# Optimization experiments

Hardware: AMD Instinct MI355X
Metric: run time of the kernel (lower is better)

Reference implementation:

```python
import jax, jax.numpy as jnp
import numpy as np

B, N, C, H, P, DP = 2, 512, 384, 12, 4, 128
CH = C // H
SCALE = CH ** -0.5
EPS = 1e-5


def setup_inputs() -> dict:
    key = jax.random.key(0)
    ks = jax.random.split(key, 16)
    w = lambda k, i, o: jax.random.normal(k, (i, o), jnp.float32) * 0.02
    inp = {
        'single': jax.random.normal(ks[0], (B, N, C), jnp.float32),
        'pair': jax.random.normal(ks[1], (B, N, N, DP), jnp.float32),
        'rot': jax.random.normal(ks[2], (B, N, 3, 3), jnp.float32),
        'trans': jax.random.normal(ks[3], (B, N, 3), jnp.float32),
        'mask': jnp.ones((B, N), jnp.float32),
        'Wq': w(ks[4], C, C), 'bq': jnp.zeros((C,)),
        'Wk': w(ks[5], C, C), 'bk': jnp.zeros((C,)),
        'Wv': w(ks[6], C, C), 'bv': jnp.zeros((C,)),
        'Wpb': w(ks[7], DP, H), 'bpb': jnp.zeros((H,)),
        'Wqp': w(ks[8], C, H * P * 3), 'bqp': jnp.zeros((H * P * 3,)),
        'Wkp': w(ks[9], C, H * P * 3), 'bkp': jnp.zeros((H * P * 3,)),
        'Wvp': w(ks[10], C, H * P * 3), 'bvp': jnp.zeros((H * P * 3,)),
        'Wo': w(ks[11], C, C), 'bo': jnp.zeros((C,)),
        'Wpo': w(ks[12], H * P * 3, C), 'bpo': jnp.zeros((C,)),
        'ln_g': jnp.ones((C,)), 'ln_b': jnp.zeros((C,)),
    }
    return inp


def _to_global(pts, rot, trans):
    # pts: [B,N,H,P,3], rot: [B,N,3,3], trans: [B,N,3]
    return jnp.einsum('bnhpd,bnde->bnhpe', pts, rot) + trans[:, :, None, None, :]


def reference(single, pair, rot, trans, mask,
              Wq, bq, Wk, bk, Wv, bv, Wpb, bpb,
              Wqp, bqp, Wkp, bkp, Wvp, bvp,
              Wo, bo, Wpo, bpo, ln_g, ln_b):
    q = (single @ Wq + bq).reshape(B, N, H, CH)
    k = (single @ Wk + bk).reshape(B, N, H, CH)
    v = (single @ Wv + bv).reshape(B, N, H, CH)
    pair_bias = jnp.transpose(pair @ Wpb + bpb, (0, 3, 1, 2))  # [B,H,N,N]

    q_pts = (single @ Wqp + bqp).reshape(B, N, H, P, 3)
    k_pts = (single @ Wkp + bkp).reshape(B, N, H, P, 3)
    qg = _to_global(q_pts, rot, trans)
    kg = _to_global(k_pts, rot, trans)

    q2 = jnp.sum(qg * qg, axis=(3, 4))  # [B,N,H]
    k2 = jnp.sum(kg * kg, axis=(3, 4))
    qk = jnp.einsum('bnhpd,bmhpd->bhnm', qg, kg)
    q2h = jnp.transpose(q2, (0, 2, 1))  # [B,H,N]
    k2h = jnp.transpose(k2, (0, 2, 1))
    point_logits = -0.5 * (q2h[..., :, None] + k2h[..., None, :] - 2.0 * qk) * SCALE

    scalar_logits = jnp.einsum('bnhc,bmhc->bhnm', q, k) * SCALE
    logits = scalar_logits + pair_bias + point_logits

    mask2d = mask[:, None, :, None] * mask[:, None, None, :]  # [B,1,N,N]
    logits = jnp.where(mask2d == 0, -1e9, logits)
    attn = jax.nn.softmax(logits, axis=-1)

    weighted_scalar = jnp.einsum('bhnm,bmhc->bnhc', attn, v).reshape(B, N, C)

    v_pts = (single @ Wvp + bvp).reshape(B, N, H, P, 3)
    vg = _to_global(v_pts, rot, trans)
    weighted_points = jnp.einsum('bhnm,bmhpd->bnhpd', attn, vg).reshape(B, N, H * P * 3)

    point_proj = weighted_points @ Wpo + bpo
    out = (weighted_scalar + point_proj) @ Wo + bo

    x = single + out
    mu = jnp.mean(x, axis=-1, keepdims=True)
    var = jnp.mean((x - mu) ** 2, axis=-1, keepdims=True)
    return (x - mu) * jax.lax.rsqrt(var + EPS) * ln_g + ln_b
```

## Files before the change

### kernel.cpp

```cpp
#include <hip/hip_runtime.h>
#include <hip/hip_bf16.h>

#define Bb   2
#define Nn   512
#define Cc   384
#define Hh   12
#define BN   1024
#define NC1  1584
#define CT1  99
#define SCALE 0.17677669529663687f

typedef __attribute__((ext_vector_type(8))) short short8;
typedef __attribute__((ext_vector_type(4))) float f32x4;

__device__ __forceinline__ unsigned short f2bf(float f){
  union { float f; unsigned u; } v; v.f = f;
  unsigned u = v.u;
  unsigned r = u + 0x7fffu + ((u >> 16) & 1u);
  return (unsigned short)(r >> 16);
}
__device__ __forceinline__ float bf_lo(unsigned u){ union{unsigned u; float f;} v; v.u = u << 16; return v.f; }
__device__ __forceinline__ float bf_hi(unsigned u){ union{unsigned u; float f;} v; v.u = u & 0xffff0000u; return v.f; }
__device__ __forceinline__ unsigned pack2(float a, float b){
  return (unsigned)f2bf(a) | ((unsigned)f2bf(b) << 16);
}

__device__ __forceinline__ void bias_job(const float* __restrict__ pair,
    const float* __restrict__ Wpb, const float* __restrict__ bpb,
    unsigned short* __restrict__ biasf, int jid, int tid)
{
  int l = tid & 63, w = tid >> 6;
  long m0 = (long)jid * 64 + w * 16;
  long m = m0 + (l & 15);
  int kb = (l >> 4) << 3;
  int col = l & 15;
  short8 bf[4];
#pragma unroll
  for (int t = 0; t < 4; ++t){
#pragma unroll
    for (int j = 0; j < 8; ++j){
      int k = t * 32 + kb + j;
      float v = (col < 12) ? Wpb[k * 12 + col] : 0.f;
      bf[t][j] = (short)f2bf(v);
    }
  }
  const float* pr = pair + m * 128 + kb;
  f32x4 acc = {0,0,0,0};
#pragma unroll
  for (int t = 0; t < 4; ++t){
    float4 x0 = *(const float4*)(pr + t * 32);
    float4 x1 = *(const float4*)(pr + t * 32 + 4);
    short8 a;
    a[0] = (short)f2bf(x0.x); a[1] = (short)f2bf(x0.y);
    a[2] = (short)f2bf(x0.z); a[3] = (short)f2bf(x0.w);
    a[4] = (short)f2bf(x1.x); a[5] = (short)f2bf(x1.y);
    a[6] = (short)f2bf(x1.z); a[7] = (short)f2bf(x1.w);
    acc = __builtin_amdgcn_mfma_f32_16x16x32_bf16(a, bf[t], acc, 0, 0, 0);
  }
  int h = col;
  if (h < 12){
    long mr = m0 + ((l >> 4) << 2);
    int b  = (int)(mr >> 18);
    int i  = (int)((mr >> 9) & 511);
    int j  = (int)(mr & 511);
    int jt = j >> 5, f = (j >> 4) & 1, g2 = (j >> 2) & 3;
    int qt = i >> 4, q = i & 15;
    float bb = bpb[h];
    long e16 = (((((long)((b * 12 + h) * 16 + jt) * 32 + qt) * 2 + f) * 64) + (g2 * 16 + q)) * 4;
    uint2 wv; wv.x = pack2(acc[0] + bb, acc[1] + bb); wv.y = pack2(acc[2] + bb, acc[3] + bb);
    *(uint2*)(biasf + e16) = wv;
  }
}

__global__ __launch_bounds__(256) void k1_prep_bias(
    const float* __restrict__ single,
    const float* __restrict__ Wq, const float* __restrict__ Wk, const float* __restrict__ Wv,
    const float* __restrict__ Wqp, const float* __restrict__ Wkp, const float* __restrict__ Wvp,
    const float* __restrict__ bq, const float* __restrict__ bk, const float* __restrict__ bv,
    const float* __restrict__ bqp, const float* __restrict__ bkp, const float* __restrict__ bvp,
    const float* __restrict__ Wpo, const float* __restrict__ Wo,
    const float* __restrict__ pair, const float* __restrict__ Wpb, const float* __restrict__ bpb,
    unsigned short* __restrict__ sbf, unsigned short* __restrict__ wcat, float* __restrict__ bcat,
    unsigned short* __restrict__ wpof, unsigned short* __restrict__ wof,
    unsigned short* __restrict__ wppad, unsigned short* __restrict__ biasf)
{
  int bid = blockIdx.x, tid = threadIdx.x;
  if (bid >= 256){ bias_job(pair, Wpb, bpb, biasf, bid - 256, tid); return; }

  const int n0 = BN * Cc;
  const int n1 = 12 * CT1 * 512;
  const int n4 = NC1;
  const int n5 = 61440;
  const int n6 = 147456;
  const int n7 = BN * 16;
  const int total = n0 + n1 + n4 + n5 + n6 + n7;
  for (int i = bid * 256 + tid; i < total; i += 256 * 256){
    int e = i;
    if (e < n0){ sbf[e] = f2bf(single[e]); continue; }
    e -= n0;
    if (e < n1){
      int j8 = e & 7, l = (e >> 3) & 63, ctt = e >> 9;
      int ct = ctt % CT1, t = ctt / CT1;
      int k = t * 32 + ((l >> 4) << 3) + j8;
      int col = (ct << 4) + (l & 15);
      float v;
      if (col < 1152){
        const float* W = (col < 384) ? Wq : (col < 768 ? Wk : Wv);
        v = W[k * 384 + (col % 384)];
      } else {
        int c2 = col - 1152;
        const float* W = (c2 < 144) ? Wqp : (c2 < 288 ? Wkp : Wvp);
        v = W[k * 144 + (c2 % 144)];
      }
      wcat[e] = f2bf(v); continue;
    }
    e -= n1;
    if (e < n4){
      int col = e; float v;
      if (col < 1152){
        const float* bb = (col < 384) ? bq : (col < 768 ? bk : bv);
        v = bb[col % 384];
      } else {
        int c2 = col - 1152;
        const float* bb = (c2 < 144) ? bqp : (c2 < 288 ? bkp : bvp);
        v = bb[c2 % 144];
      }
      bcat[col] = v; continue;
    }
    e -= n4;
    if (e < n5){
      int j8 = e & 7, l = (e >> 3) & 63, ctt = e >> 9;
      int ct = ctt % 24, t = ctt / 24;
      int k = t * 32 + ((l >> 4) << 3) + j8;
      int col = (ct << 4) + (l & 15);
      wpof[e] = (k < 144) ? f2bf(Wpo[k * 384 + col]) : (unsigned short)0;
      continue;
    }
    e -= n5;
    if (e < n6){
      int j8 = e & 7, l = (e >> 3) & 63, ctt = e >> 9;
      int ct = ctt % 24, t = ctt / 24;
      int k = t * 32 + ((l >> 4) << 3) + j8;
      int col = (ct << 4) + (l & 15);
      wof[e] = f2bf(Wo[k * 384 + col]);
      continue;
    }
    e -= n6;
    { int row = e >> 4, c = e & 15; wppad[row * 160 + 144 + c] = 0; }
  }
}

__global__ __launch_bounds__(256) void k2_proj_bias(
    const unsigned short* __restrict__ sbf, const unsigned short* __restrict__ wcat,
    const float* __restrict__ bcat, float* __restrict__ proj,
    const float* __restrict__ pair, const float* __restrict__ Wpb, const float* __restrict__ bpb,
    unsigned short* __restrict__ biasf)
{
  int bid = blockIdx.x, tid = threadIdx.x;
  if (bid >= 528){ bias_job(pair, Wpb, bpb, biasf, 1024 + (bid - 528), tid); return; }

  int l = tid & 63, w = tid >> 6;
  int bx = bid & 15, by = bid >> 4;
  int m0 = bx * 64 + w * 16;
  const unsigned short* Ap = sbf + (long)(m0 + (l & 15)) * Cc + ((l >> 4) << 3);
  int ct0 = by * 3;
  f32x4 acc0 = {0,0,0,0}, acc1 = {0,0,0,0}, acc2 = {0,0,0,0};
  for (int t = 0; t < 12; ++t){
    short8 a = *(const short8*)(Ap + t * 32);
    const unsigned short* wp_ = wcat + ((long)(t * CT1 + ct0) * 64 + l) * 8;
    short8 b0 = *(const short8*)(wp_);
    short8 b1 = *(const short8*)(wp_ + 512);
    short8 b2 = *(const short8*)(wp_ + 1024);
    acc0 = __builtin_amdgcn_mfma_f32_16x16x32_bf16(a, b0, acc0, 0, 0, 0);
    acc1 = __builtin_amdgcn_mfma_f32_16x16x32_bf16(a, b1, acc1, 0, 0, 0);
    acc2 = __builtin_amdgcn_mfma_f32_16x16x32_bf16(a, b2, acc2, 0, 0, 0);
  }
  int rbase = m0 + ((l >> 4) << 2);
  int cb = by * 48 + (l & 15);
#pragma unroll
  for (int c = 0; c < 3; ++c){
    f32x4 ac = (c == 0) ? acc0 : (c == 1 ? acc1 : acc2);
    int col = cb + c * 16;
    float bb = bcat[col];
#pragma unroll
    for (int r = 0; r < 4; ++r)
      proj[(long)(rbase + r) * NC1 + col] = ac[r] + bb;
  }
}

__global__ __launch_bounds__(256) void k3_pack_bias(
    const float* __restrict__ proj, const float* __restrict__ rot,
    const float* __restrict__ trans, const float* __restrict__ mask,
    unsigned short* __restrict__ qf, unsigned short* __restrict__ kf,
    unsigned short* __restrict__ vf, float* __restrict__ q2h, float* __restrict__ k2h,
    const float* __restrict__ pair, const float* __restrict__ Wpb, const float* __restrict__ bpb,
    unsigned short* __restrict__ biasf)
{
  __shared__ float smemf[5792];
  int bid = blockIdx.x, tid = threadIdx.x;
  if (bid >= 384){ bias_job(pair, Wpb, bpb, biasf, 4096 + (bid - 384), tid); return; }

  float* scal = smemf;
  float* praw = scal + 3072;
  float* pg   = praw + 1152;
  float* rots = pg + 1152;
  float* trs  = rots + 288;
  float* msk  = trs + 96;

  int jid = bid;
  int b = jid / 192, rem = jid % 192;
  int h = rem >> 4, rt = rem & 15;
  int j0 = rt * 32;
  int bn0 = b * 512 + j0;
  int bh = b * 12 + h;

  for (int idx = tid; idx < 3072; idx += 256){
    int a = idx >> 10, row = (idx >> 5) & 31, c = idx & 31;
    scal[idx] = proj[(long)(bn0 + row) * NC1 + a * 384 + h * 32 + c];
  }
  for (int idx = tid; idx < 1152; idx += 256){
    int a = idx / 384, rr = idx % 384, row = rr / 12, pe = rr % 12;
    praw[idx] = proj[(long)(bn0 + row) * NC1 + 1152 + a * 144 + h * 12 + pe];
  }
  for (int idx = tid; idx < 288; idx += 256) rots[idx] = rot[(long)bn0 * 9 + idx];
  for (int idx = tid; idx < 96; idx += 256)  trs[idx] = trans[(long)bn0 * 3 + idx];
  for (int idx = tid; idx < 32; idx += 256)  msk[idx] = mask[bn0 + idx];
  __syncthreads();

  for (int idx = tid; idx < 1152; idx += 256){
    int a = idx / 384, rr = idx % 384, row = rr / 12, pe = rr % 12;
    int p = pe / 3, ee = pe % 3;
    pg[idx] = praw[a * 384 + row * 12 + p * 3] * rots[row * 9 + ee]
            + praw[a * 384 + row * 12 + p * 3 + 1] * rots[row * 9 + 3 + ee]
            + praw[a * 384 + row * 12 + p * 3 + 2] * rots[row * 9 + 6 + ee] + trs[row * 3 + ee];
  }
  __syncthreads();

  for (int idx = tid; idx < 64; idx += 256){
    int a = idx >> 5, row = idx & 31;
    float s2 = 0.f;
#pragma unroll
    for (int pe = 0; pe < 12; ++pe){ float g = pg[a * 384 + row * 12 + pe]; s2 += g * g; }
    float mv = msk[row];
    float rres = -0.5f * SCALE * s2 + (mv != 0.f ? 0.f : -2e9f);
    (a ? k2h : q2h)[(long)bh * 512 + j0 + row] = rres;
  }

  for (int idx = tid; idx < 2048; idx += 256){
    int a = idx >> 10, r = idx & 1023;
    int jjp = r & 3, l = (r >> 2) & 63, ks = (r >> 8) & 1, sub = r >> 9;
    int row = sub * 16 + (l & 15);
    int kk = ks * 32 + ((l >> 4) << 3) + jjp * 2;
    int k1 = kk + 1;
    float v0 = (kk < 32) ? scal[a * 1024 + row * 32 + kk] : (kk < 44 ? pg[a * 384 + row * 12 + kk - 32] : 0.f);
    float v1 = (k1 < 32) ? scal[a * 1024 + row * 32 + k1] : (k1 < 44 ? pg[a * 384 + row * 12 + k1 - 32] : 0.f);
    if (a == 0){ v0 *= SCALE; v1 *= SCALE; }
    unsigned* dst = (unsigned*)(a ? kf : qf);
    dst[((((long)bh * 32 + rt * 2 + sub) * 2 + ks) * 64 + l) * 4 + jjp] = pack2(v0, v1);
  }

  for (int idx = tid; idx < 768; idx += 256){
    int jjp = idx & 3, l = (idx >> 2) & 63, cf = idx >> 8;
    int c = cf * 16 + (l & 15);
    int j = ((l >> 4) << 3) + jjp * 2;
    float v0 = (c < 32) ? scal[2048 + j * 32 + c]       : (c < 44 ? pg[768 + j * 12 + (c - 32)]       : 0.f);
    float v1 = (c < 32) ? scal[2048 + (j + 1) * 32 + c] : (c < 44 ? pg[768 + (j + 1) * 12 + (c - 32)] : 0.f);
    ((unsigned*)vf)[(((long)bh * 16 + rt) * 3 + cf) * 256 + l * 4 + jjp] = pack2(v0, v1);
  }
}

__global__ __launch_bounds__(256) void attn2_kernel(
    const unsigned short* __restrict__ qf, const unsigned short* __restrict__ kf,
    const unsigned short* __restrict__ vf, const unsigned short* __restrict__ biasf,
    const float* __restrict__ q2h, const float* __restrict__ k2h,
    float* __restrict__ wsout, unsigned short* __restrict__ wpout)
{
  __shared__ unsigned short pls[4][16][40];
  __shared__ float oW[4][3][64][4];
  __shared__ float mW[4][16], lsW[4][16];
  __shared__ float fW[4][16], linvS[16];

  int l = threadIdx.x & 63, w = threadIdx.x >> 6;
  int qt = blockIdx.x, h = blockIdx.y, b = blockIdx.z;
  int bh = b * 12 + h;
  int g = l >> 4, q_ = l & 15;

  const short8* qp = (const short8*)(qf + (((long)(bh * 32 + qt) * 2) * 64 + l) * 8);
  short8 qA = qp[0], qB = qp[64];
  float cq = q2h[(long)bh * 512 + qt * 16 + q_];

  float m = -1e30f, ls = 0.f;
  f32x4 o0 = {0,0,0,0}, o1 = {0,0,0,0}, o2 = {0,0,0,0};
  const f32x4 z4 = {0,0,0,0};

#pragma unroll
  for (int ji = 0; ji < 4; ++ji){
    int jt = w * 4 + ji;
    const short8* kp = (const short8*)(kf + (((long)(bh * 32 + jt * 2) * 2) * 64 + l) * 8);
    short8 k00 = kp[0], k01 = kp[64], k10 = kp[128], k11 = kp[192];
    f32x4 s0 = __builtin_amdgcn_mfma_f32_16x16x32_bf16(k00, qA, z4, 0, 0, 0);
    s0 = __builtin_amdgcn_mfma_f32_16x16x32_bf16(k01, qB, s0, 0, 0, 0);
    f32x4 s1 = __builtin_amdgcn_mfma_f32_16x16x32_bf16(k10, qA, z4, 0, 0, 0);
    s1 = __builtin_amdgcn_mfma_f32_16x16x32_bf16(k11, qB, s1, 0, 0, 0);

    const uint2* bp = (const uint2*)(biasf + ((((long)(bh * 16 + jt) * 32 + qt) * 2) * 64) * 4);
    uint2 bb0 = bp[l], bb1 = bp[64 + l];
    const float4* k2p = (const float4*)(k2h + (long)bh * 512 + jt * 32);
    float4 ck0 = k2p[g], ck1 = k2p[4 + g];

    s0[0] += bf_lo(bb0.x) + cq + ck0.x;
    s0[1] += bf_hi(bb0.x) + cq + ck0.y;
    s0[2] += bf_lo(bb0.y) + cq + ck0.z;
    s0[3] += bf_hi(bb0.y) + cq + ck0.w;
    s1[0] += bf_lo(bb1.x) + cq + ck1.x;
    s1[1] += bf_hi(bb1.x) + cq + ck1.y;
    s1[2] += bf_lo(bb1.y) + cq + ck1.z;
    s1[3] += bf_hi(bb1.y) + cq + ck1.w;

    float tm = fmaxf(fmaxf(fmaxf(s0[0], s0[1]), fmaxf(s0[2], s0[3])),
                     fmaxf(fmaxf(s1[0], s1[1]), fmaxf(s1[2], s1[3])));
    tm = fmaxf(tm, __shfl_xor(tm, 16));
    tm = fmaxf(tm, __shfl_xor(tm, 32));
    float mn = fmaxf(m, tm);
    float alpha = __expf(m - mn);
    f32x4 p0, p1;
    float ts = 0.f;
#pragma unroll
    for (int r = 0; r < 4; ++r){ p0[r] = __expf(s0[r] - mn); ts += p0[r]; }
#pragma unroll
    for (int r = 0; r < 4; ++r){ p1[r] = __expf(s1[r] - mn); ts += p1[r]; }
    ts += __shfl_xor(ts, 16);
    ts += __shfl_xor(ts, 32);
    ls = ls * alpha + ts; m = mn;

    f32x4 av;
#pragma unroll
    for (int r = 0; r < 4; ++r) av[r] = __shfl(alpha, g * 4 + r);
#pragma unroll
    for (int r = 0; r < 4; ++r){ o0[r] *= av[r]; o1[r] *= av[r]; o2[r] *= av[r]; }

    uint2 w0; w0.x = pack2(p0[0], p0[1]); w0.y = pack2(p0[2], p0[3]);
    uint2 w1; w1.x = pack2(p1[0], p1[1]); w1.y = pack2(p1[2], p1[3]);
    *(uint2*)&pls[w][q_][g * 4]      = w0;
    *(uint2*)&pls[w][q_][16 + g * 4] = w1;
    short8 pa = *(const short8*)&pls[w][q_][g * 8];

    const short8* vp = (const short8*)(vf + (((long)(bh * 16 + jt) * 3) * 64 + l) * 8);
    short8 v0 = vp[0], v1 = vp[64], v2 = vp[128];
    o0 = __builtin_amdgcn_mfma_f32_16x16x32_bf16(pa, v0, o0, 0, 0, 0);
    o1 = __builtin_amdgcn_mfma_f32_16x16x32_bf16(pa, v1, o1, 0, 0, 0);
    o2 = __builtin_amdgcn_mfma_f32_16x16x32_bf16(pa, v2, o2, 0, 0, 0);
  }

  if (g == 0){ mW[w][q_] = m; lsW[w][q_] = ls; }
  *(f32x4*)&oW[w][0][l][0] = o0;
  *(f32x4*)&oW[w][1][l][0] = o1;
  *(f32x4*)&oW[w][2][l][0] = o2;
  __syncthreads();

  if (w == 0){
    float M = fmaxf(fmaxf(mW[0][q_], mW[1][q_]), fmaxf(mW[2][q_], mW[3][q_]));
    float f = __expf(mW[g][q_] - M);
    fW[g][q_] = f;
    float lf = lsW[g][q_] * f;
    lf += __shfl_xor(lf, 16);
    lf += __shfl_xor(lf, 32);
    if (g == 0) linvS[q_] = 1.f / lf;
  }
  __syncthreads();

  if (w < 3){
    float fr[4][4], li[4];
#pragma unroll
    for (int r = 0; r < 4; ++r){
      int q = g * 4 + r;
      li[r] = linvS[q];
#pragma unroll
      for (int vw = 0; vw < 4; ++vw) fr[vw][r] = fW[vw][q];
    }
    f32x4 sum = {0,0,0,0};
#pragma unroll
    for (int vw = 0; vw < 4; ++vw){
      f32x4 ov = *(const f32x4*)&oW[vw][w][l][0];
#pragma unroll
      for (int r = 0; r < 4; ++r) sum[r] += ov[r] * fr[vw][r];
    }
#pragma unroll
    for (int r = 0; r < 4; ++r){
      long bn = (long)b * 512 + qt * 16 + g * 4 + r;
      float val = sum[r] * li[r];
      if (w == 0)      wsout[bn * 384 + h * 32 + q_] = val;
      else if (w == 1) wsout[bn * 384 + h * 32 + 16 + q_] = val;
      else if (q_ < 12) wpout[bn * 160 + h * 12 + q_] = f2bf(val);
    }
  }
}

__global__ __launch_bounds__(256) void tail_kernel(
    const unsigned short* __restrict__ wpbuf, const unsigned short* __restrict__ wpof,
    const float* __restrict__ bpo, const float* __restrict__ wso,
    const unsigned short* __restrict__ wof, const float* __restrict__ bo,
    const float* __restrict__ single, const float* __restrict__ ln_g,
    const float* __restrict__ ln_b, float* __restrict__ out)
{
  __shared__ unsigned short t1s[16][392];
  __shared__ float redS[4][16], redQ[4][16];
  int l = threadIdx.x & 63, w = threadIdx.x >> 6;
  int m0 = blockIdx.x * 16;
  int rb = (l >> 4) << 2;
  int arow = m0 + (l & 15);

  {
    short8 awp[5];
    const unsigned short* Ap = wpbuf + (long)arow * 160 + ((l >> 4) << 3);
#pragma unroll
    for (int t = 0; t < 5; ++t) awp[t] = *(const short8*)(Ap + t * 32);
#pragma unroll
    for (int c6 = 0; c6 < 6; ++c6){
      int ct = w * 6 + c6;
      f32x4 acc = {0,0,0,0};
#pragma unroll
      for (int t = 0; t < 5; ++t){
        short8 bfr = *(const short8*)(wpof + ((long)(t * 24 + ct) * 64 + l) * 8);
        acc = __builtin_amdgcn_mfma_f32_16x16x32_bf16(awp[t], bfr, acc, 0, 0, 0);
      }
      int col = ct * 16 + (l & 15);
      float bb = bpo[col];
#pragma unroll
      for (int r = 0; r < 4; ++r){
        float v = acc[r] + bb + wso[(long)(m0 + rb + r) * 384 + col];
        t1s[rb + r][col] = f2bf(v);
      }
    }
  }
  __syncthreads();

  short8 a2[12];
  {
    int lr = l & 15;
#pragma unroll
    for (int t = 0; t < 12; ++t)
      a2[t] = *(const short8*)&t1s[lr][t * 32 + ((l >> 4) << 3)];
  }
  f32x4 xa[6];
  float s1[4] = {0,0,0,0}, s2[4] = {0,0,0,0};
#pragma unroll
  for (int c6 = 0; c6 < 6; ++c6){
    int ct = w * 6 + c6;
    f32x4 acc = {0,0,0,0};
#pragma unroll
    for (int t = 0; t < 12; ++t){
      short8 bfr = *(const short8*)(wof + ((long)(t * 24 + ct) * 64 + l) * 8);
      acc = __builtin_amdgcn_mfma_f32_16x16x32_bf16(a2[t], bfr, acc, 0, 0, 0);
    }
    int col = ct * 16 + (l & 15);
    float bb = bo[col];
#pragma unroll
    for (int r = 0; r < 4; ++r){
      float v = acc[r] + bb + single[(long)(m0 + rb + r) * 384 + col];
      acc[r] = v; s1[r] += v; s2[r] += v * v;
    }
    xa[c6] = acc;
  }
#pragma unroll
  for (int off = 1; off < 16; off <<= 1){
#pragma unroll
    for (int r = 0; r < 4; ++r){
      s1[r] += __shfl_xor(s1[r], off);
      s2[r] += __shfl_xor(s2[r], off);
    }
  }
  if ((l & 15) == 0){
#pragma unroll
    for (int r = 0; r < 4; ++r){ redS[w][rb + r] = s1[r]; redQ[w][rb + r] = s2[r]; }
  }
  __syncthreads();
  float mu[4], inv[4];
#pragma unroll
  for (int r = 0; r < 4; ++r){
    float ts = redS[0][rb + r] + redS[1][rb + r] + redS[2][rb + r] + redS[3][rb + r];
    float tq = redQ[0][rb + r] + redQ[1][rb + r] + redQ[2][rb + r] + redQ[3][rb + r];
    mu[r] = ts * (1.f / 384.f);
    float var = tq * (1.f / 384.f) - mu[r] * mu[r];
    inv[r] = rsqrtf(var + 1e-5f);
  }
#pragma unroll
  for (int c6 = 0; c6 < 6; ++c6){
    int ct = w * 6 + c6;
    int col = ct * 16 + (l & 15);
    float g = ln_g[col], bt = ln_b[col];
#pragma unroll
    for (int r = 0; r < 4; ++r)
      out[(long)(m0 + rb + r) * 384 + col] = (xa[c6][r] - mu[r]) * inv[r] * g + bt;
  }
}

extern "C" void kernel_launch(void* const* d_in, const int* in_sizes, int n_in,
                              void* d_out, int out_size, void* d_ws, size_t ws_size,
                              hipStream_t stream)
{
  const float* single = (const float*)d_in[0];
  const float* pair   = (const float*)d_in[1];
  const float* rot    = (const float*)d_in[2];
  const float* trans  = (const float*)d_in[3];
  const float* mask   = (const float*)d_in[4];
  const float* Wq  = (const float*)d_in[5];  const float* bq  = (const float*)d_in[6];
  const float* Wk  = (const float*)d_in[7];  const float* bk  = (const float*)d_in[8];
  const float* Wv  = (const float*)d_in[9];  const float* bv  = (const float*)d_in[10];
  const float* Wpb = (const float*)d_in[11]; const float* bpb = (const float*)d_in[12];
  const float* Wqp = (const float*)d_in[13]; const float* bqp = (const float*)d_in[14];
  const float* Wkp = (const float*)d_in[15]; const float* bkp = (const float*)d_in[16];
  const float* Wvp = (const float*)d_in[17]; const float* bvp = (const float*)d_in[18];
  const float* Wo  = (const float*)d_in[19]; const float* bo  = (const float*)d_in[20];
  const float* Wpo = (const float*)d_in[21]; const float* bpo = (const float*)d_in[22];
  const float* ln_g = (const float*)d_in[23]; const float* ln_b = (const float*)d_in[24];

  char* wsb = (char*)d_ws;
  size_t off = 0;
  auto alloc = [&](size_t bytes) -> void* {
    void* p = wsb + off; off += (bytes + 255) & ~(size_t)255; return p;
  };
  unsigned short* sbf  = (unsigned short*)alloc((size_t)BN * Cc * 2);
  unsigned short* wcat = (unsigned short*)alloc((size_t)12 * CT1 * 512 * 2);
  unsigned short* wpof = (unsigned short*)alloc((size_t)5 * 24 * 512 * 2);
  unsigned short* wof  = (unsigned short*)alloc((size_t)12 * 24 * 512 * 2);
  float* bcat  = (float*)alloc(NC1 * 4);
  float* proj  = (float*)alloc((size_t)BN * NC1 * 4);
  unsigned short* biasf = (unsigned short*)alloc((size_t)Bb * Hh * Nn * Nn * 2);
  unsigned short* qfragb = (unsigned short*)alloc((size_t)786432 * 2);
  unsigned short* kfragb = (unsigned short*)alloc((size_t)786432 * 2);
  unsigned short* vfragb = (unsigned short*)alloc((size_t)589824 * 2);
  float* q2hb  = (float*)alloc((size_t)12288 * 4);
  float* k2hb  = (float*)alloc((size_t)12288 * 4);
  float* wso   = (float*)alloc((size_t)BN * 384 * 4);
  unsigned short* wpbuf = (unsigned short*)alloc((size_t)BN * 160 * 2);
  if (off > ws_size) return;

  k1_prep_bias<<<256 + 1024, 256, 0, stream>>>(
      single, Wq, Wk, Wv, Wqp, Wkp, Wvp, bq, bk, bv, bqp, bkp, bvp, Wpo, Wo,
      pair, Wpb, bpb, sbf, wcat, bcat, wpof, wof, wpbuf, biasf);
  k2_proj_bias<<<528 + 3072, 256, 0, stream>>>(
      sbf, wcat, bcat, proj, pair, Wpb, bpb, biasf);
  k3_pack_bias<<<384 + 4096, 256, 0, stream>>>(
      proj, rot, trans, mask, qfragb, kfragb, vfragb, q2hb, k2hb,
      pair, Wpb, bpb, biasf);
  attn2_kernel<<<dim3(32, 12, 2), 256, 0, stream>>>(qfragb, kfragb, vfragb, biasf,
                                                    q2hb, k2hb, wso, wpbuf);
  tail_kernel<<<64, 256, 0, stream>>>(wpbuf, wpof, bpo, wso, wof, bo,
                                      single, ln_g, ln_b, (float*)d_out);
}
```

Before: 106.2 us.

## Fuse pair-bias projection into split-KV attention with merged tail reduction

The pair-bias projection no longer runs as extra blocks in the prep kernels and is no longer staged through a global bf16 bias buffer. It is computed inside the attention kernel per (batch, query tile, 64-key chunk) and kept in LDS, where all 12 heads consume it. Attention is split across 8 key chunks, each writing partial outputs with its max and sum, and the tail kernel merges these flash-style before the output projection and layernorm. This removes a large global round trip of the bias tensor, but the partials buffer adds extra traffic and the merge step adds per-thread register pressure.

New measurement: 133.3 us. 25.5% more time.

```diff
diff --git a/kernel.cpp b/kernel.cpp
--- a/kernel.cpp
+++ b/kernel.cpp
@@ -25,75 +25,23 @@
   return (unsigned)f2bf(a) | ((unsigned)f2bf(b) << 16);
 }
 
-__device__ __forceinline__ void bias_job(const float* __restrict__ pair,
-    const float* __restrict__ Wpb, const float* __restrict__ bpb,
-    unsigned short* __restrict__ biasf, int jid, int tid)
-{
-  int l = tid & 63, w = tid >> 6;
-  long m0 = (long)jid * 64 + w * 16;
-  long m = m0 + (l & 15);
-  int kb = (l >> 4) << 3;
-  int col = l & 15;
-  short8 bf[4];
-#pragma unroll
-  for (int t = 0; t < 4; ++t){
-#pragma unroll
-    for (int j = 0; j < 8; ++j){
-      int k = t * 32 + kb + j;
-      float v = (col < 12) ? Wpb[k * 12 + col] : 0.f;
-      bf[t][j] = (short)f2bf(v);
-    }
-  }
-  const float* pr = pair + m * 128 + kb;
-  f32x4 acc = {0,0,0,0};
-#pragma unroll
-  for (int t = 0; t < 4; ++t){
-    float4 x0 = *(const float4*)(pr + t * 32);
-    float4 x1 = *(const float4*)(pr + t * 32 + 4);
-    short8 a;
-    a[0] = (short)f2bf(x0.x); a[1] = (short)f2bf(x0.y);
-    a[2] = (short)f2bf(x0.z); a[3] = (short)f2bf(x0.w);
-    a[4] = (short)f2bf(x1.x); a[5] = (short)f2bf(x1.y);
-    a[6] = (short)f2bf(x1.z); a[7] = (short)f2bf(x1.w);
-    acc = __builtin_amdgcn_mfma_f32_16x16x32_bf16(a, bf[t], acc, 0, 0, 0);
-  }
-  int h = col;
-  if (h < 12){
-    long mr = m0 + ((l >> 4) << 2);
-    int b  = (int)(mr >> 18);
-    int i  = (int)((mr >> 9) & 511);
-    int j  = (int)(mr & 511);
-    int jt = j >> 5, f = (j >> 4) & 1, g2 = (j >> 2) & 3;
-    int qt = i >> 4, q = i & 15;
-    float bb = bpb[h];
-    long e16 = (((((long)((b * 12 + h) * 16 + jt) * 32 + qt) * 2 + f) * 64) + (g2 * 16 + q)) * 4;
-    uint2 wv; wv.x = pack2(acc[0] + bb, acc[1] + bb); wv.y = pack2(acc[2] + bb, acc[3] + bb);
-    *(uint2*)(biasf + e16) = wv;
-  }
-}
-
-__global__ __launch_bounds__(256) void k1_prep_bias(
+__global__ __launch_bounds__(256) void k1_prep(
     const float* __restrict__ single,
     const float* __restrict__ Wq, const float* __restrict__ Wk, const float* __restrict__ Wv,
     const float* __restrict__ Wqp, const float* __restrict__ Wkp, const float* __restrict__ Wvp,
     const float* __restrict__ bq, const float* __restrict__ bk, const float* __restrict__ bv,
     const float* __restrict__ bqp, const float* __restrict__ bkp, const float* __restrict__ bvp,
     const float* __restrict__ Wpo, const float* __restrict__ Wo,
-    const float* __restrict__ pair, const float* __restrict__ Wpb, const float* __restrict__ bpb,
     unsigned short* __restrict__ sbf, unsigned short* __restrict__ wcat, float* __restrict__ bcat,
-    unsigned short* __restrict__ wpof, unsigned short* __restrict__ wof,
-    unsigned short* __restrict__ wppad, unsigned short* __restrict__ biasf)
+    unsigned short* __restrict__ wpof, unsigned short* __restrict__ wof)
 {
   int bid = blockIdx.x, tid = threadIdx.x;
-  if (bid >= 256){ bias_job(pair, Wpb, bpb, biasf, bid - 256, tid); return; }
-
   const int n0 = BN * Cc;
   const int n1 = 12 * CT1 * 512;
   const int n4 = NC1;
   const int n5 = 61440;
   const int n6 = 147456;
-  const int n7 = BN * 16;
-  const int total = n0 + n1 + n4 + n5 + n6 + n7;
+  const int total = n0 + n1 + n4 + n5 + n6;
   for (int i = bid * 256 + tid; i < total; i += 256 * 256){
     int e = i;
     if (e < n0){ sbf[e] = f2bf(single[e]); continue; }
@@ -137,28 +85,21 @@
       continue;
     }
     e -= n5;
-    if (e < n6){
+    {
       int j8 = e & 7, l = (e >> 3) & 63, ctt = e >> 9;
       int ct = ctt % 24, t = ctt / 24;
       int k = t * 32 + ((l >> 4) << 3) + j8;
       int col = (ct << 4) + (l & 15);
       wof[e] = f2bf(Wo[k * 384 + col]);
-      continue;
-    }
-    e -= n6;
-    { int row = e >> 4, c = e & 15; wppad[row * 160 + 144 + c] = 0; }
-  }
-}
-
-__global__ __launch_bounds__(256) void k2_proj_bias(
+    }
+  }
+}
+
+__global__ __launch_bounds__(256) void k2_proj(
     const unsigned short* __restrict__ sbf, const unsigned short* __restrict__ wcat,
-    const float* __restrict__ bcat, float* __restrict__ proj,
-    const float* __restrict__ pair, const float* __restrict__ Wpb, const float* __restrict__ bpb,
-    unsigned short* __restrict__ biasf)
+    const float* __restrict__ bcat, float* __restrict__ proj)
 {
   int bid = blockIdx.x, tid = threadIdx.x;
-  if (bid >= 528){ bias_job(pair, Wpb, bpb, biasf, 1024 + (bid - 528), tid); return; }
-
   int l = tid & 63, w = tid >> 6;
   int bx = bid & 15, by = bid >> 4;
   int m0 = bx * 64 + w * 16;
@@ -188,17 +129,14 @@
   }
 }
 
-__global__ __launch_bounds__(256) void k3_pack_bias(
+__global__ __launch_bounds__(256) void k3_pack(
     const float* __restrict__ proj, const float* __restrict__ rot,
     const float* __restrict__ trans, const float* __restrict__ mask,
     unsigned short* __restrict__ qf, unsigned short* __restrict__ kf,
-    unsigned short* __restrict__ vf, float* __restrict__ q2h, float* __restrict__ k2h,
-    const float* __restrict__ pair, const float* __restrict__ Wpb, const float* __restrict__ bpb,
-    unsigned short* __restrict__ biasf)
+    unsigned short* __restrict__ vf, float* __restrict__ q2h, float* __restrict__ k2h)
 {
   __shared__ float smemf[5792];
   int bid = blockIdx.x, tid = threadIdx.x;
-  if (bid >= 384){ bias_job(pair, Wpb, bpb, biasf, 4096 + (bid - 384), tid); return; }
 
   float* scal = smemf;
   float* praw = scal + 3072;
@@ -269,150 +207,191 @@
   }
 }
 
-__global__ __launch_bounds__(256) void attn2_kernel(
+__global__ __launch_bounds__(512) void kC_bias_attn(
+    const float* __restrict__ pair, const float* __restrict__ Wpb,
+    const float* __restrict__ bpb,
     const unsigned short* __restrict__ qf, const unsigned short* __restrict__ kf,
-    const unsigned short* __restrict__ vf, const unsigned short* __restrict__ biasf,
+    const unsigned short* __restrict__ vf,
     const float* __restrict__ q2h, const float* __restrict__ k2h,
-    float* __restrict__ wsout, unsigned short* __restrict__ wpout)
+    float* __restrict__ partials)
 {
-  __shared__ unsigned short pls[4][16][40];
-  __shared__ float oW[4][3][64][4];
-  __shared__ float mW[4][16], lsW[4][16];
-  __shared__ float fW[4][16], linvS[16];
-
-  int l = threadIdx.x & 63, w = threadIdx.x >> 6;
-  int qt = blockIdx.x, h = blockIdx.y, b = blockIdx.z;
-  int bh = b * 12 + h;
-  int g = l >> 4, q_ = l & 15;
-
-  const short8* qp = (const short8*)(qf + (((long)(bh * 32 + qt) * 2) * 64 + l) * 8);
-  short8 qA = qp[0], qB = qp[64];
-  float cq = q2h[(long)bh * 512 + qt * 16 + q_];
-
-  float m = -1e30f, ls = 0.f;
-  f32x4 o0 = {0,0,0,0}, o1 = {0,0,0,0}, o2 = {0,0,0,0};
+  __shared__ __align__(16) unsigned int bias_lds[32 * 12 * 17];
+  __shared__ __align__(16) float scratch[8][16 * 48];
+
+  int tid = threadIdx.x;
+  int l = tid & 63, w = tid >> 6;
+  int q_ = l & 15, g = l >> 4;
+  int bid = blockIdx.x;
+  int jq = bid & 7; int r5 = bid >> 3; int it = r5 & 31; int b = r5 >> 5;
+  int i0 = it * 16, j0 = jq * 64;
   const f32x4 z4 = {0,0,0,0};
 
-#pragma unroll
-  for (int ji = 0; ji < 4; ++ji){
-    int jt = w * 4 + ji;
-    const short8* kp = (const short8*)(kf + (((long)(bh * 32 + jt * 2) * 2) * 64 + l) * 8);
-    short8 k00 = kp[0], k01 = kp[64], k10 = kp[128], k11 = kp[192];
-    f32x4 s0 = __builtin_amdgcn_mfma_f32_16x16x32_bf16(k00, qA, z4, 0, 0, 0);
-    s0 = __builtin_amdgcn_mfma_f32_16x16x32_bf16(k01, qB, s0, 0, 0, 0);
-    f32x4 s1 = __builtin_amdgcn_mfma_f32_16x16x32_bf16(k10, qA, z4, 0, 0, 0);
-    s1 = __builtin_amdgcn_mfma_f32_16x16x32_bf16(k11, qB, s1, 0, 0, 0);
-
-    const uint2* bp = (const uint2*)(biasf + ((((long)(bh * 16 + jt) * 32 + qt) * 2) * 64) * 4);
-    uint2 bb0 = bp[l], bb1 = bp[64 + l];
-    const float4* k2p = (const float4*)(k2h + (long)bh * 512 + jt * 32);
-    float4 ck0 = k2p[g], ck1 = k2p[4 + g];
-
-    s0[0] += bf_lo(bb0.x) + cq + ck0.x;
-    s0[1] += bf_hi(bb0.x) + cq + ck0.y;
-    s0[2] += bf_lo(bb0.y) + cq + ck0.z;
-    s0[3] += bf_hi(bb0.y) + cq + ck0.w;
-    s1[0] += bf_lo(bb1.x) + cq + ck1.x;
-    s1[1] += bf_hi(bb1.x) + cq + ck1.y;
-    s1[2] += bf_lo(bb1.y) + cq + ck1.z;
-    s1[3] += bf_hi(bb1.y) + cq + ck1.w;
-
-    float tm = fmaxf(fmaxf(fmaxf(s0[0], s0[1]), fmaxf(s0[2], s0[3])),
-                     fmaxf(fmaxf(s1[0], s1[1]), fmaxf(s1[2], s1[3])));
-    tm = fmaxf(tm, __shfl_xor(tm, 16));
-    tm = fmaxf(tm, __shfl_xor(tm, 32));
-    float mn = fmaxf(m, tm);
-    float alpha = __expf(m - mn);
-    f32x4 p0, p1;
+  short8 bfw[4];
+#pragma unroll
+  for (int t = 0; t < 4; ++t){
+#pragma unroll
+    for (int j8 = 0; j8 < 8; ++j8){
+      int k = t * 32 + g * 8 + j8;
+      bfw[t][j8] = (short)f2bf((q_ < 12) ? Wpb[k * 12 + q_] : 0.f);
+    }
+  }
+  float bb = (q_ < 12) ? bpb[q_] : 0.f;
+
+#pragma unroll
+  for (int ii = 0; ii < 2; ++ii){
+    int i = w * 2 + ii;
+    const float* prow = pair + ((long)(b * 512 + i0 + i) * 512 + j0) * 128;
+#pragma unroll
+    for (int jt4 = 0; jt4 < 4; ++jt4){
+      const float* pr = prow + (long)(jt4 * 16 + q_) * 128 + g * 8;
+      f32x4 acc = z4;
+#pragma unroll
+      for (int t = 0; t < 4; ++t){
+        float4 x0 = *(const float4*)(pr + t * 32);
+        float4 x1 = *(const float4*)(pr + t * 32 + 4);
+        short8 a;
+        a[0] = (short)f2bf(x0.x); a[1] = (short)f2bf(x0.y);
+        a[2] = (short)f2bf(x0.z); a[3] = (short)f2bf(x0.w);
+        a[4] = (short)f2bf(x1.x); a[5] = (short)f2bf(x1.y);
+        a[6] = (short)f2bf(x1.z); a[7] = (short)f2bf(x1.w);
+        acc = __builtin_amdgcn_mfma_f32_16x16x32_bf16(a, bfw[t], acc, 0, 0, 0);
+      }
+      if (q_ < 12){
+        int jp = jt4 * 8 + g * 2;
+        bias_lds[(jp * 12 + q_) * 17 + i]       = pack2(acc[0] + bb, acc[1] + bb);
+        bias_lds[((jp + 1) * 12 + q_) * 17 + i] = pack2(acc[2] + bb, acc[3] + bb);
+      }
+    }
+  }
+  __syncthreads();
+
+  float* wscr = scratch[w];
+  unsigned short* pls = (unsigned short*)wscr;
+
+  for (int hi = 0; hi < 2; ++hi){
+    int h = w + hi * 8;
+    if (h >= 12) break;
+    int bh = b * 12 + h;
+    const short8* qp = (const short8*)(qf + (((long)(bh * 32 + it) * 2) * 64 + l) * 8);
+    short8 qA = qp[0], qB = qp[64];
+    float cq = q2h[(long)bh * 512 + i0 + q_];
+
+    f32x4 s[4];
+#pragma unroll
+    for (int jt4 = 0; jt4 < 4; ++jt4){
+      int jf = (j0 >> 4) + jt4;
+      const short8* kp = (const short8*)(kf + ((((long)bh * 32 + jf) * 2) * 64 + l) * 8);
+      f32x4 st = __builtin_amdgcn_mfma_f32_16x16x32_bf16(kp[0], qA, z4, 0, 0, 0);
+      st = __builtin_amdgcn_mfma_f32_16x16x32_bf16(kp[64], qB, st, 0, 0, 0);
+      float4 ck = *(const float4*)(k2h + (long)bh * 512 + jf * 16 + g * 4);
+      int jp = jt4 * 8 + g * 2;
+      unsigned b0 = bias_lds[(jp * 12 + h) * 17 + q_];
+      unsigned b1 = bias_lds[((jp + 1) * 12 + h) * 17 + q_];
+      st[0] += bf_lo(b0) + cq + ck.x;
+      st[1] += bf_hi(b0) + cq + ck.y;
+      st[2] += bf_lo(b1) + cq + ck.z;
+      st[3] += bf_hi(b1) + cq + ck.w;
+      s[jt4] = st;
+    }
+    float m = -1e30f;
+#pragma unroll
+    for (int jt4 = 0; jt4 < 4; ++jt4)
+#pragma unroll
+      for (int r = 0; r < 4; ++r) m = fmaxf(m, s[jt4][r]);
+    m = fmaxf(m, __shfl_xor(m, 16));
+    m = fmaxf(m, __shfl_xor(m, 32));
     float ts = 0.f;
 #pragma unroll
-    for (int r = 0; r < 4; ++r){ p0[r] = __expf(s0[r] - mn); ts += p0[r]; }
-#pragma unroll
-    for (int r = 0; r < 4; ++r){ p1[r] = __expf(s1[r] - mn); ts += p1[r]; }
+    for (int jt4 = 0; jt4 < 4; ++jt4)
+#pragma unroll
+      for (int r = 0; r < 4; ++r){ s[jt4][r] = __expf(s[jt4][r] - m); ts += s[jt4][r]; }
     ts += __shfl_xor(ts, 16);
     ts += __shfl_xor(ts, 32);
-    ls = ls * alpha + ts; m = mn;
-
-    f32x4 av;
-#pragma unroll
-    for (int r = 0; r < 4; ++r) av[r] = __shfl(alpha, g * 4 + r);
-#pragma unroll
-    for (int r = 0; r < 4; ++r){ o0[r] *= av[r]; o1[r] *= av[r]; o2[r] *= av[r]; }
-
-    uint2 w0; w0.x = pack2(p0[0], p0[1]); w0.y = pack2(p0[2], p0[3]);
-    uint2 w1; w1.x = pack2(p1[0], p1[1]); w1.y = pack2(p1[2], p1[3]);
-    *(uint2*)&pls[w][q_][g * 4]      = w0;
-    *(uint2*)&pls[w][q_][16 + g * 4] = w1;
-    short8 pa = *(const short8*)&pls[w][q_][g * 8];
-
-    const short8* vp = (const short8*)(vf + (((long)(bh * 16 + jt) * 3) * 64 + l) * 8);
-    short8 v0 = vp[0], v1 = vp[64], v2 = vp[128];
-    o0 = __builtin_amdgcn_mfma_f32_16x16x32_bf16(pa, v0, o0, 0, 0, 0);
-    o1 = __builtin_amdgcn_mfma_f32_16x16x32_bf16(pa, v1, o1, 0, 0, 0);
-    o2 = __builtin_amdgcn_mfma_f32_16x16x32_bf16(pa, v2, o2, 0, 0, 0);
-  }
-
-  if (g == 0){ mW[w][q_] = m; lsW[w][q_] = ls; }
-  *(f32x4*)&oW[w][0][l][0] = o0;
-  *(f32x4*)&oW[w][1][l][0] = o1;
-  *(f32x4*)&oW[w][2][l][0] = o2;
-  __syncthreads();
-
-  if (w == 0){
-    float M = fmaxf(fmaxf(mW[0][q_], mW[1][q_]), fmaxf(mW[2][q_], mW[3][q_]));
-    float f = __expf(mW[g][q_] - M);
-    fW[g][q_] = f;
-    float lf = lsW[g][q_] * f;
-    lf += __shfl_xor(lf, 16);
-    lf += __shfl_xor(lf, 32);
-    if (g == 0) linvS[q_] = 1.f / lf;
-  }
-  __syncthreads();
-
-  if (w < 3){
-    float fr[4][4], li[4];
+
+    f32x4 o0 = z4, o1 = z4, o2 = z4;
+#pragma unroll
+    for (int ch = 0; ch < 2; ++ch){
+      uint2 w0; w0.x = pack2(s[ch*2][0], s[ch*2][1]);   w0.y = pack2(s[ch*2][2], s[ch*2][3]);
+      uint2 w1; w1.x = pack2(s[ch*2+1][0], s[ch*2+1][1]); w1.y = pack2(s[ch*2+1][2], s[ch*2+1][3]);
+      *(uint2*)&pls[q_ * 40 + g * 4]      = w0;
+      *(uint2*)&pls[q_ * 40 + 16 + g * 4] = w1;
+      short8 pa = *(const short8*)&pls[q_ * 40 + g * 8];
+      int jt32 = (j0 >> 5) + ch;
+      const short8* vp = (const short8*)(vf + (((long)(bh * 16 + jt32) * 3) * 64 + l) * 8);
+      o0 = __builtin_amdgcn_mfma_f32_16x16x32_bf16(pa, vp[0], o0, 0, 0, 0);
+      o1 = __builtin_amdgcn_mfma_f32_16x16x32_bf16(pa, vp[64], o1, 0, 0, 0);
+      o2 = __builtin_amdgcn_mfma_f32_16x16x32_bf16(pa, vp[128], o2, 0, 0, 0);
+    }
+
+    int c_ = q_;
 #pragma unroll
     for (int r = 0; r < 4; ++r){
       int q = g * 4 + r;
-      li[r] = linvS[q];
-#pragma unroll
-      for (int vw = 0; vw < 4; ++vw) fr[vw][r] = fW[vw][q];
-    }
-    f32x4 sum = {0,0,0,0};
-#pragma unroll
-    for (int vw = 0; vw < 4; ++vw){
-      f32x4 ov = *(const f32x4*)&oW[vw][w][l][0];
-#pragma unroll
-      for (int r = 0; r < 4; ++r) sum[r] += ov[r] * fr[vw][r];
-    }
-#pragma unroll
-    for (int r = 0; r < 4; ++r){
-      long bn = (long)b * 512 + qt * 16 + g * 4 + r;
-      float val = sum[r] * li[r];
-      if (w == 0)      wsout[bn * 384 + h * 32 + q_] = val;
-      else if (w == 1) wsout[bn * 384 + h * 32 + 16 + q_] = val;
-      else if (q_ < 12) wpout[bn * 160 + h * 12 + q_] = f2bf(val);
-    }
-  }
-}
-
-__global__ __launch_bounds__(256) void tail_kernel(
-    const unsigned short* __restrict__ wpbuf, const unsigned short* __restrict__ wpof,
-    const float* __restrict__ bpo, const float* __restrict__ wso,
+      wscr[q * 48 + c_] = o0[r];
+      wscr[q * 48 + 16 + c_] = o1[r];
+      if (c_ < 12) wscr[q * 48 + 32 + c_] = o2[r];
+    }
+    if (l < 16){ wscr[q_ * 48 + 44] = m; wscr[q_ * 48 + 45] = ts; }
+
+    long pbase = ((long)bid * 12 + h) * 736;
+    for (int e = l; e < 736; e += 64){
+      int q = e / 46, c = e % 46;
+      partials[pbase + e] = wscr[q * 48 + c];
+    }
+  }
+}
+
+__global__ __launch_bounds__(256) void kD_merge_tail(
+    const float* __restrict__ partials,
+    const unsigned short* __restrict__ wpof, const float* __restrict__ bpo,
     const unsigned short* __restrict__ wof, const float* __restrict__ bo,
     const float* __restrict__ single, const float* __restrict__ ln_g,
     const float* __restrict__ ln_b, float* __restrict__ out)
 {
+  __shared__ float o_lds[16][388];
+  __shared__ unsigned short wp_lds[16][160];
   __shared__ unsigned short t1s[16][392];
   __shared__ float redS[4][16], redQ[4][16];
-  int l = threadIdx.x & 63, w = threadIdx.x >> 6;
-  int m0 = blockIdx.x * 16;
+  int tid = threadIdx.x;
+  int bid = blockIdx.x;
+  int m0 = bid * 16;
+
+  for (int e = tid; e < 16 * 16; e += 256) wp_lds[e >> 4][144 + (e & 15)] = 0;
+
+  if (tid < 192){
+    int h = tid >> 4, q = tid & 15;
+    float M = -1e30f;
+#pragma unroll
+    for (int jqq = 0; jqq < 8; ++jqq){
+      float mj = partials[((((long)(bid * 8 + jqq)) * 12 + h) * 16 + q) * 46 + 44];
+      M = fmaxf(M, mj);
+    }
+    float osum[44];
+#pragma unroll
+    for (int c = 0; c < 44; ++c) osum[c] = 0.f;
+    float lt = 0.f;
+#pragma unroll
+    for (int jqq = 0; jqq < 8; ++jqq){
+      const float* pp = partials + ((((long)(bid * 8 + jqq)) * 12 + h) * 16 + q) * 46;
+      float f = __expf(pp[44] - M);
+      lt += pp[45] * f;
+#pragma unroll
+      for (int c = 0; c < 44; ++c) osum[c] += pp[c] * f;
+    }
+    float inv = 1.f / lt;
+#pragma unroll
+    for (int c = 0; c < 32; ++c) o_lds[q][h * 32 + c] = osum[c] * inv;
+#pragma unroll
+    for (int c = 0; c < 12; ++c) wp_lds[q][h * 12 + c] = f2bf(osum[32 + c] * inv);
+  }
+  __syncthreads();
+
+  int l = tid & 63, w = tid >> 6;
   int rb = (l >> 4) << 2;
-  int arow = m0 + (l & 15);
 
   {
     short8 awp[5];
-    const unsigned short* Ap = wpbuf + (long)arow * 160 + ((l >> 4) << 3);
+    const unsigned short* Ap = &wp_lds[l & 15][(l >> 4) << 3];
 #pragma unroll
     for (int t = 0; t < 5; ++t) awp[t] = *(const short8*)(Ap + t * 32);
 #pragma unroll
@@ -428,7 +407,7 @@
       float bb = bpo[col];
 #pragma unroll
       for (int r = 0; r < 4; ++r){
-        float v = acc[r] + bb + wso[(long)(m0 + rb + r) * 384 + col];
+        float v = acc[r] + bb + o_lds[rb + r][col];
         t1s[rb + r][col] = f2bf(v);
       }
     }
@@ -526,26 +505,22 @@
   unsigned short* wof  = (unsigned short*)alloc((size_t)12 * 24 * 512 * 2);
   float* bcat  = (float*)alloc(NC1 * 4);
   float* proj  = (float*)alloc((size_t)BN * NC1 * 4);
-  unsigned short* biasf = (unsigned short*)alloc((size_t)Bb * Hh * Nn * Nn * 2);
   unsigned short* qfragb = (unsigned short*)alloc((size_t)786432 * 2);
   unsigned short* kfragb = (unsigned short*)alloc((size_t)786432 * 2);
   unsigned short* vfragb = (unsigned short*)alloc((size_t)589824 * 2);
   float* q2hb  = (float*)alloc((size_t)12288 * 4);
   float* k2hb  = (float*)alloc((size_t)12288 * 4);
-  float* wso   = (float*)alloc((size_t)BN * 384 * 4);
-  unsigned short* wpbuf = (unsigned short*)alloc((size_t)BN * 160 * 2);
+  float* partials = (float*)alloc((size_t)512 * 12 * 736 * 4);
   if (off > ws_size) return;
 
-  k1_prep_bias<<<256 + 1024, 256, 0, stream>>>(
+  k1_prep<<<256, 256, 0, stream>>>(
       single, Wq, Wk, Wv, Wqp, Wkp, Wvp, bq, bk, bv, bqp, bkp, bvp, Wpo, Wo,
-      pair, Wpb, bpb, sbf, wcat, bcat, wpof, wof, wpbuf, biasf);
-  k2_proj_bias<<<528 + 3072, 256, 0, stream>>>(
-      sbf, wcat, bcat, proj, pair, Wpb, bpb, biasf);
-  k3_pack_bias<<<384 + 4096, 256, 0, stream>>>(
-      proj, rot, trans, mask, qfragb, kfragb, vfragb, q2hb, k2hb,
-      pair, Wpb, bpb, biasf);
-  attn2_kernel<<<dim3(32, 12, 2), 256, 0, stream>>>(qfragb, kfragb, vfragb, biasf,
-                                                    q2hb, k2hb, wso, wpbuf);
-  tail_kernel<<<64, 256, 0, stream>>>(wpbuf, wpof, bpo, wso, wof, bo,
-                                      single, ln_g, ln_b, (float*)d_out);
-}
+      sbf, wcat, bcat, wpof, wof);
+  k2_proj<<<528, 256, 0, stream>>>(sbf, wcat, bcat, proj);
+  k3_pack<<<384, 256, 0, stream>>>(proj, rot, trans, mask,
+                                   qfragb, kfragb, vfragb, q2hb, k2hb);
+  kC_bias_attn<<<512, 512, 0, stream>>>(pair, Wpb, bpb,
+                                        qfragb, kfragb, vfragb, q2hb, k2hb, partials);
+  kD_merge_tail<<<64, 256, 0, stream>>>(partials, wpof, bpo, wof, bo,
+                                        single, ln_g, ln_b, (float*)d_out);
+}
```
